# Kernel optimization log

Hardware: AMD Instinct MI355X
Metric: run time of the kernel (lower is better)

Reference implementation:

```python
import jax, jax.numpy as jnp
import numpy as np

NF4_LUT = jnp.array([-1.0, -0.6961928009986877, -0.5250730514526367, -0.39491719007492065,
                     -0.28444138169288635, -0.18477343022823334, -0.08820830285549164, 0.0,
                     0.07107656449079514, 0.14263366162776947, 0.22430233657360077,
                     0.3203405737876892, 0.4407068192958832, 0.5905631184577942,
                     0.796090841293335, 1.0], dtype=jnp.float32)

BLOCK_SIZE = 64
OUT_FEATURES = 11008
IN_FEATURES = 4096


def dequantize_nf4(packed, absmax, out_shape):
    # packed: (O, I//2) int codes 0..255; absmax: (O, num_blocks)
    higher = packed // 16
    lower = packed % 16
    unpacked = jnp.stack([lower, higher], axis=-1).reshape(out_shape)  # (O, I)
    dequant = NF4_LUT[unpacked]  # LUT gather -> fp32 (O, I)
    O, I = out_shape
    # block-wise absmax scale
    dequant = (dequant.reshape(O, I // BLOCK_SIZE, BLOCK_SIZE) * absmax[:, :, None]).reshape(O, I)
    return dequant


def setup_inputs() -> dict:
    key = jax.random.key(0)
    k1, k2, k3, k4 = jax.random.split(key, 4)
    x = jax.random.normal(k1, (4, 2048, IN_FEATURES), dtype=jnp.float32)
    weight = jax.random.randint(k2, (OUT_FEATURES, IN_FEATURES // 2), 0, 256, dtype=jnp.int32)
    absmax = jax.random.uniform(k3, (OUT_FEATURES, IN_FEATURES // BLOCK_SIZE), dtype=jnp.float32)
    bias = jax.random.normal(k4, (OUT_FEATURES,), dtype=jnp.float32)
    return {"x": x, "weight": weight, "absmax": absmax, "bias": bias}


def reference(x, weight, absmax, bias):
    w = dequantize_nf4(weight, absmax, (OUT_FEATURES, IN_FEATURES))  # (O, I)
    # F.linear: y = x @ w.T + bias
    return jnp.einsum('bsi,oi->bso', x, w) + bias
```

## Files before the change

### kernel.cpp

```cpp
#include <hip/hip_runtime.h>

#define IN_F 4096
#define OUT_F 11008

typedef __attribute__((ext_vector_type(8))) short bf16x8;
typedef __attribute__((ext_vector_type(4))) float f32x4;
typedef __attribute__((ext_vector_type(4))) unsigned short us4;
typedef __attribute__((ext_vector_type(8))) unsigned short us8;

__device__ __forceinline__ unsigned short f2bf(float f) {
  unsigned int u = __float_as_uint(f);
  u += 0x7FFFu + ((u >> 16) & 1u);
  return (unsigned short)(u >> 16);
}

__global__ __launch_bounds__(256) void cvt_x(const float* __restrict__ X,
                                             unsigned short* __restrict__ Xb, int n8) {
  for (int i = blockIdx.x * blockDim.x + threadIdx.x; i < n8;
       i += gridDim.x * blockDim.x) {
    const float4 a = reinterpret_cast<const float4*>(X)[2 * i];
    const float4 b = reinterpret_cast<const float4*>(X)[2 * i + 1];
    us8 h;
    h[0] = f2bf(a.x); h[1] = f2bf(a.y); h[2] = f2bf(a.z); h[3] = f2bf(a.w);
    h[4] = f2bf(b.x); h[5] = f2bf(b.y); h[6] = f2bf(b.z); h[7] = f2bf(b.w);
    reinterpret_cast<us8*>(Xb)[i] = h;
  }
}

__global__ __launch_bounds__(256) void dequant_w(const int* __restrict__ Wp,
                                                 const float* __restrict__ Amax,
                                                 unsigned short* __restrict__ Wb, int n4) {
  __shared__ float lutS[16];
  if (threadIdx.x < 16) {
    const float lut[16] = {-1.0f, -0.6961928009986877f, -0.5250730514526367f,
        -0.39491719007492065f, -0.28444138169288635f, -0.18477343022823334f,
        -0.08820830285549164f, 0.0f, 0.07107656449079514f, 0.14263366162776947f,
        0.22430233657360077f, 0.3203405737876892f, 0.4407068192958832f,
        0.5905631184577942f, 0.796090841293335f, 1.0f};
    lutS[threadIdx.x] = lut[threadIdx.x];
  }
  __syncthreads();
  for (int i = blockIdx.x * blockDim.x + threadIdx.x; i < n4;
       i += gridDim.x * blockDim.x) {
    const int j = i * 4;
    const int row = j >> 11;
    const int coli = j & 2047;
    const float am = Amax[row * (IN_F / 64) + (coli >> 5)];
    const int4 pk = reinterpret_cast<const int4*>(Wp)[i];
    us8 h; int c;
    c = pk.x & 255; h[0] = f2bf(lutS[c & 15] * am); h[1] = f2bf(lutS[c >> 4] * am);
    c = pk.y & 255; h[2] = f2bf(lutS[c & 15] * am); h[3] = f2bf(lutS[c >> 4] * am);
    c = pk.z & 255; h[4] = f2bf(lutS[c & 15] * am); h[5] = f2bf(lutS[c >> 4] * am);
    c = pk.w & 255; h[6] = f2bf(lutS[c & 15] * am); h[7] = f2bf(lutS[c >> 4] * am);
    reinterpret_cast<us8*>(Wb)[i] = h;
  }
}

#define MF(a, b, c) __builtin_amdgcn_mfma_f32_16x16x32_bf16(a, b, c, 0, 0, 0)
#define GLDS(src, dst) __builtin_amdgcn_global_load_lds( \
    (const __attribute__((address_space(1))) void*)(src), \
    (__attribute__((address_space(3))) void*)(dst), 16, 0, 0)
#define FENCE asm volatile("" ::: "memory")
#define BAR do { FENCE; __builtin_amdgcn_s_barrier(); FENCE; } while (0)
#define VM0 asm volatile("s_waitcnt vmcnt(0)" ::: "memory")
#define P1 __builtin_amdgcn_s_setprio(1)
#define P0 __builtin_amdgcn_s_setprio(0)

__global__ __launch_bounds__(512, 2) void gemm256(
    const unsigned short* __restrict__ A,
    const unsigned short* __restrict__ B,
    const float* __restrict__ Bias, float* __restrict__ Out, int M) {
  extern __shared__ unsigned short sm[];
  char* const smc = (char*)sm;

  const int tid = threadIdx.x;
  const int l = tid & 63;
  const int wid = tid >> 6;

  const int Nb = OUT_F / 256;

  const int bps = 16 * Nb;
  const int pxc = bps >> 3;
  const int i6 = (int)blockIdx.x % bps;
  const int sup = (int)blockIdx.x / bps;
  const int k = (i6 & 7) * pxc + (i6 >> 3);
  const int m0 = (sup * 16 + (k & 15)) * 256;
  const int n0 = (k >> 4) * 256;

  const int lv = (l & 15) * 64 + (((l >> 4) ^ ((l >> 1) & 3)) * 16);
  const int aLane = (wid >> 2) * 8192 + lv;
  const int bLane = 32768 + (wid & 3) * 4096 + lv;

  const int rq = tid >> 2;
  const int cs = (tid & 3) ^ ((tid >> 3) & 3);
  const unsigned short* gAs = A + (size_t)(m0 + rq) * IN_F + cs * 8;
  const unsigned short* gBs = B + (size_t)(n0 + rq) * IN_F + cs * 8;

#define SA(t, kh) do { \
    unsigned short* d_ = sm + (size_t)((((t) & 1) * 4096) + (kh) * 1024 + wid * 64) * 8; \
    const unsigned short* s_ = gAs + (size_t)(t) * 64 + (kh) * 32; \
    GLDS(s_, d_); GLDS(s_ + 524288, d_ + 4096); } while (0)
#define SB(t, kh) do { \
    unsigned short* d_ = sm + (size_t)((((t) & 1) * 4096) + 2048 + (kh) * 1024 + wid * 64) * 8; \
    const unsigned short* s_ = gBs + (size_t)(t) * 64 + (kh) * 32; \
    GLDS(s_, d_); GLDS(s_ + 4096, d_ + 4096); } while (0)
#undef SB
#define SB(t, kh) do { \
    unsigned short* d_ = sm + (size_t)((((t) & 1) * 4096) + 2048 + (kh) * 1024 + wid * 64) * 8; \
    const unsigned short* s_ = gBs + (size_t)(t) * 64 + (kh) * 32; \
    GLDS(s_, d_); GLDS(s_ + 524288, d_ + 4096); } while (0)

#define MM32(AA0, AA1, AA2, AA3, AA4, AA5, AA6, AA7, BB0, BB1, BB2, BB3) do { \
    acc[0][0]=MF(AA0,BB0,acc[0][0]); acc[0][1]=MF(AA0,BB1,acc[0][1]); \
    acc[0][2]=MF(AA0,BB2,acc[0][2]); acc[0][3]=MF(AA0,BB3,acc[0][3]); \
    acc[1][0]=MF(AA1,BB0,acc[1][0]); acc[1][1]=MF(AA1,BB1,acc[1][1]); \
    acc[1][2]=MF(AA1,BB2,acc[1][2]); acc[1][3]=MF(AA1,BB3,acc[1][3]); \
    acc[2][0]=MF(AA2,BB0,acc[2][0]); acc[2][1]=MF(AA2,BB1,acc[2][1]); \
    acc[2][2]=MF(AA2,BB2,acc[2][2]); acc[2][3]=MF(AA2,BB3,acc[2][3]); \
    acc[3][0]=MF(AA3,BB0,acc[3][0]); acc[3][1]=MF(AA3,BB1,acc[3][1]); \
    acc[3][2]=MF(AA3,BB2,acc[3][2]); acc[3][3]=MF(AA3,BB3,acc[3][3]); \
    acc[4][0]=MF(AA4,BB0,acc[4][0]); acc[4][1]=MF(AA4,BB1,acc[4][1]); \
    acc[4][2]=MF(AA4,BB2,acc[4][2]); acc[4][3]=MF(AA4,BB3,acc[4][3]); \
    acc[5][0]=MF(AA5,BB0,acc[5][0]); acc[5][1]=MF(AA5,BB1,acc[5][1]); \
    acc[5][2]=MF(AA5,BB2,acc[5][2]); acc[5][3]=MF(AA5,BB3,acc[5][3]); \
    acc[6][0]=MF(AA6,BB0,acc[6][0]); acc[6][1]=MF(AA6,BB1,acc[6][1]); \
    acc[6][2]=MF(AA6,BB2,acc[6][2]); acc[6][3]=MF(AA6,BB3,acc[6][3]); \
    acc[7][0]=MF(AA7,BB0,acc[7][0]); acc[7][1]=MF(AA7,BB1,acc[7][1]); \
    acc[7][2]=MF(AA7,BB2,acc[7][2]); acc[7][3]=MF(AA7,BB3,acc[7][3]); } while (0)

#define KTILE(T, STG) do { \
    VM0; \
    BAR; \
    const char* LAb = smc + (((T) & 1) << 16) + aLane; \
    const char* LBb = smc + (((T) & 1) << 16) + bLane; \
    bf16x8 x0, x1, x2, x3, x4, x5, x6, x7, y0, y1, y2, y3; \
    bf16x8 u0, u1, u2, u3, u4, u5, u6, u7, v0, v1, v2, v3; \
    y0 = *(const bf16x8*)(LBb);        y1 = *(const bf16x8*)(LBb + 1024); \
    y2 = *(const bf16x8*)(LBb + 2048); y3 = *(const bf16x8*)(LBb + 3072); \
    x0 = *(const bf16x8*)(LAb);        x1 = *(const bf16x8*)(LAb + 1024); \
    x2 = *(const bf16x8*)(LAb + 2048); x3 = *(const bf16x8*)(LAb + 3072); \
    x4 = *(const bf16x8*)(LAb + 4096); x5 = *(const bf16x8*)(LAb + 5120); \
    x6 = *(const bf16x8*)(LAb + 6144); x7 = *(const bf16x8*)(LAb + 7168); \
    v0 = *(const bf16x8*)(LBb + 16384);        v1 = *(const bf16x8*)(LBb + 16384 + 1024); \
    v2 = *(const bf16x8*)(LBb + 16384 + 2048); v3 = *(const bf16x8*)(LBb + 16384 + 3072); \
    u0 = *(const bf16x8*)(LAb + 16384);        u1 = *(const bf16x8*)(LAb + 16384 + 1024); \
    u2 = *(const bf16x8*)(LAb + 16384 + 2048); u3 = *(const bf16x8*)(LAb + 16384 + 3072); \
    u4 = *(const bf16x8*)(LAb + 16384 + 4096); u5 = *(const bf16x8*)(LAb + 16384 + 5120); \
    u6 = *(const bf16x8*)(LAb + 16384 + 6144); u7 = *(const bf16x8*)(LAb + 16384 + 7168); \
    if (STG) { SA((T) + 1, 0); SB((T) + 1, 0); SA((T) + 1, 1); SB((T) + 1, 1); } \
    P1; MM32(x0, x1, x2, x3, x4, x5, x6, x7, y0, y1, y2, y3); P0; \
    P1; MM32(u0, u1, u2, u3, u4, u5, u6, u7, v0, v1, v2, v3); P0; \
  } while (0)

  f32x4 acc[8][4];
#pragma unroll
  for (int i = 0; i < 8; ++i)
#pragma unroll
    for (int j = 0; j < 4; ++j) acc[i][j] = {0.f, 0.f, 0.f, 0.f};

  SA(0, 0); SB(0, 0); SA(0, 1); SB(0, 1);

  for (int T = 0; T < 63; ++T) { KTILE(T, 1); }
  KTILE(63, 0);

  const int crow = m0 + (wid >> 2) * 128 + ((l >> 4) << 2);
  const int ccol = n0 + (wid & 3) * 64 + (l & 15);
#pragma unroll
  for (int nf = 0; nf < 4; ++nf) {
    const float bv = Bias[ccol + nf * 16];
#pragma unroll
    for (int f = 0; f < 8; ++f)
#pragma unroll
      for (int rg = 0; rg < 4; ++rg)
        Out[(size_t)(crow + f * 16 + rg) * OUT_F + ccol + nf * 16] = acc[f][nf][rg] + bv;
  }
}

__global__ __launch_bounds__(256, 2) void nf4_gemm_fused(
    const float* __restrict__ X, const int* __restrict__ Wp,
    const float* __restrict__ Amax, const float* __restrict__ Bias,
    float* __restrict__ Out, int M) {
  __shared__ unsigned short As[128 * 64];
  __shared__ unsigned short Bs[128 * 64];
  __shared__ float lutS[16];

  const int t = threadIdx.x;
  const int l = t & 63;
  const int wid = t >> 6;

  if (t < 16) {
    const float lut[16] = {-1.0f, -0.6961928009986877f, -0.5250730514526367f,
        -0.39491719007492065f, -0.28444138169288635f, -0.18477343022823334f,
        -0.08820830285549164f, 0.0f, 0.07107656449079514f, 0.14263366162776947f,
        0.22430233657360077f, 0.3203405737876892f, 0.4407068192958832f,
        0.5905631184577942f, 0.796090841293335f, 1.0f};
    lutS[t] = lut[t];
  }

  const int ntile = OUT_F / 128;
  const int m0 = (blockIdx.x / ntile) * 128;
  const int n0 = (blockIdx.x % ntile) * 128;

  const int ar = t >> 4;
  const int ac4 = t & 15;
  const int br = t >> 3;
  const int bg = t & 7;
  const int wm = (wid >> 1) * 64;
  const int wn = (wid & 1) * 64;

  f32x4 acc[4][4];
#pragma unroll
  for (int i = 0; i < 4; ++i)
#pragma unroll
    for (int j = 0; j < 4; ++j) acc[i][j] = {0.f, 0.f, 0.f, 0.f};

  __syncthreads();

  for (int k0 = 0; k0 < IN_F; k0 += 64) {
#pragma unroll
    for (int p = 0; p < 8; ++p) {
      const int r = p * 16 + ar;
      const float4 v = *reinterpret_cast<const float4*>(
          X + (size_t)(m0 + r) * IN_F + k0 + ac4 * 4);
      us4 h;
      h[0] = f2bf(v.x); h[1] = f2bf(v.y); h[2] = f2bf(v.z); h[3] = f2bf(v.w);
      const int byte = r * 128 + ((ac4 * 8) ^ ((r & 7) << 4));
      *reinterpret_cast<us4*>(reinterpret_cast<char*>(As) + byte) = h;
    }
#pragma unroll
    for (int p = 0; p < 4; ++p) {
      const int r = p * 32 + br;
      const float amv = Amax[(size_t)(n0 + r) * (IN_F / 64) + (k0 >> 6)];
      const int4 pk = *reinterpret_cast<const int4*>(
          Wp + (size_t)(n0 + r) * (IN_F / 2) + (k0 >> 1) + bg * 4);
      us8 h;
      {
        int c;
        c = pk.x & 255; h[0] = f2bf(lutS[c & 15] * amv); h[1] = f2bf(lutS[c >> 4] * amv);
        c = pk.y & 255; h[2] = f2bf(lutS[c & 15] * amv); h[3] = f2bf(lutS[c >> 4] * amv);
        c = pk.z & 255; h[4] = f2bf(lutS[c & 15] * amv); h[5] = f2bf(lutS[c >> 4] * amv);
        c = pk.w & 255; h[6] = f2bf(lutS[c & 15] * amv); h[7] = f2bf(lutS[c >> 4] * amv);
      }
      const int byte = r * 128 + ((bg * 16) ^ ((r & 7) << 4));
      *reinterpret_cast<us8*>(reinterpret_cast<char*>(Bs) + byte) = h;
    }
    __syncthreads();

#pragma unroll
    for (int kk = 0; kk < 64; kk += 32) {
      bf16x8 af[4], bfv[4];
      const int kb = (kk + ((l >> 4) << 3)) * 2;
#pragma unroll
      for (int i = 0; i < 4; ++i) {
        const int row = wm + i * 16 + (l & 15);
        af[i] = *reinterpret_cast<const bf16x8*>(
            reinterpret_cast<const char*>(As) + row * 128 + (kb ^ ((row & 7) << 4)));
      }
#pragma unroll
      for (int j = 0; j < 4; ++j) {
        const int row = wn + j * 16 + (l & 15);
        bfv[j] = *reinterpret_cast<const bf16x8*>(
            reinterpret_cast<const char*>(Bs) + row * 128 + (kb ^ ((row & 7) << 4)));
      }
#pragma unroll
      for (int i = 0; i < 4; ++i)
#pragma unroll
        for (int j = 0; j < 4; ++j)
          acc[i][j] = __builtin_amdgcn_mfma_f32_16x16x32_bf16(af[i], bfv[j], acc[i][j], 0, 0, 0);
    }
    __syncthreads();
  }

  const int crow0 = m0 + wm + ((l >> 4) << 2);
  const int ccol0 = n0 + wn + (l & 15);
#pragma unroll
  for (int j = 0; j < 4; ++j) {
    const float bv = Bias[ccol0 + j * 16];
#pragma unroll
    for (int i = 0; i < 4; ++i)
#pragma unroll
      for (int rg = 0; rg < 4; ++rg)
        Out[(size_t)(crow0 + i * 16 + rg) * OUT_F + ccol0 + j * 16] = acc[i][j][rg] + bv;
  }
}

extern "C" void kernel_launch(void* const* d_in, const int* in_sizes, int n_in,
                              void* d_out, int out_size, void* d_ws, size_t ws_size,
                              hipStream_t stream) {
  const float* X = (const float*)d_in[0];
  const int* Wp = (const int*)d_in[1];
  const float* Amax = (const float*)d_in[2];
  const float* Bias = (const float*)d_in[3];
  float* Out = (float*)d_out;

  const int M = in_sizes[0] / IN_F;
  const size_t needX = (size_t)M * IN_F * 2;
  const size_t needW = (size_t)OUT_F * IN_F * 2;
  const int grid256 = (M / 256) * (OUT_F / 256);

  if (ws_size >= needX + needW && (M % 4096) == 0) {
    unsigned short* Xb = (unsigned short*)d_ws;
    unsigned short* Wb = Xb + (size_t)M * IN_F;
    (void)hipFuncSetAttribute(reinterpret_cast<const void*>(gemm256),
                              hipFuncAttributeMaxDynamicSharedMemorySize, 131072);
    cvt_x<<<2048, 256, 0, stream>>>(X, Xb, M * (IN_F / 8));
    dequant_w<<<2048, 256, 0, stream>>>(Wp, Amax, Wb, OUT_F * (IN_F / 8));
    gemm256<<<grid256, 512, 131072, stream>>>(Xb, Wb, Bias, Out, M);
  } else {
    const int grid = (M / 128) * (OUT_F / 128);
    nf4_gemm_fused<<<grid, 256, 0, stream>>>(X, Wp, Amax, Bias, Out, M);
  }
}
```

Before: 866.6 us.

## Interleave LDS reads, global-to-LDS staging and MFMA in four sub-phases per k-tile

```diff
diff --git a/kernel.cpp b/kernel.cpp
--- a/kernel.cpp
+++ b/kernel.cpp
@@ -62,6 +62,7 @@
     (__attribute__((address_space(3))) void*)(dst), 16, 0, 0)
 #define FENCE asm volatile("" ::: "memory")
 #define BAR do { FENCE; __builtin_amdgcn_s_barrier(); FENCE; } while (0)
+#define VM4 asm volatile("s_waitcnt vmcnt(4)" ::: "memory")
 #define VM0 asm volatile("s_waitcnt vmcnt(0)" ::: "memory")
 #define P1 __builtin_amdgcn_s_setprio(1)
 #define P0 __builtin_amdgcn_s_setprio(0)
@@ -103,53 +104,46 @@
 #define SB(t, kh) do { \
     unsigned short* d_ = sm + (size_t)((((t) & 1) * 4096) + 2048 + (kh) * 1024 + wid * 64) * 8; \
     const unsigned short* s_ = gBs + (size_t)(t) * 64 + (kh) * 32; \
-    GLDS(s_, d_); GLDS(s_ + 4096, d_ + 4096); } while (0)
-#undef SB
-#define SB(t, kh) do { \
-    unsigned short* d_ = sm + (size_t)((((t) & 1) * 4096) + 2048 + (kh) * 1024 + wid * 64) * 8; \
-    const unsigned short* s_ = gBs + (size_t)(t) * 64 + (kh) * 32; \
     GLDS(s_, d_); GLDS(s_ + 524288, d_ + 4096); } while (0)
 
-#define MM32(AA0, AA1, AA2, AA3, AA4, AA5, AA6, AA7, BB0, BB1, BB2, BB3) do { \
-    acc[0][0]=MF(AA0,BB0,acc[0][0]); acc[0][1]=MF(AA0,BB1,acc[0][1]); \
-    acc[0][2]=MF(AA0,BB2,acc[0][2]); acc[0][3]=MF(AA0,BB3,acc[0][3]); \
-    acc[1][0]=MF(AA1,BB0,acc[1][0]); acc[1][1]=MF(AA1,BB1,acc[1][1]); \
-    acc[1][2]=MF(AA1,BB2,acc[1][2]); acc[1][3]=MF(AA1,BB3,acc[1][3]); \
-    acc[2][0]=MF(AA2,BB0,acc[2][0]); acc[2][1]=MF(AA2,BB1,acc[2][1]); \
-    acc[2][2]=MF(AA2,BB2,acc[2][2]); acc[2][3]=MF(AA2,BB3,acc[2][3]); \
-    acc[3][0]=MF(AA3,BB0,acc[3][0]); acc[3][1]=MF(AA3,BB1,acc[3][1]); \
-    acc[3][2]=MF(AA3,BB2,acc[3][2]); acc[3][3]=MF(AA3,BB3,acc[3][3]); \
-    acc[4][0]=MF(AA4,BB0,acc[4][0]); acc[4][1]=MF(AA4,BB1,acc[4][1]); \
-    acc[4][2]=MF(AA4,BB2,acc[4][2]); acc[4][3]=MF(AA4,BB3,acc[4][3]); \
-    acc[5][0]=MF(AA5,BB0,acc[5][0]); acc[5][1]=MF(AA5,BB1,acc[5][1]); \
-    acc[5][2]=MF(AA5,BB2,acc[5][2]); acc[5][3]=MF(AA5,BB3,acc[5][3]); \
-    acc[6][0]=MF(AA6,BB0,acc[6][0]); acc[6][1]=MF(AA6,BB1,acc[6][1]); \
-    acc[6][2]=MF(AA6,BB2,acc[6][2]); acc[6][3]=MF(AA6,BB3,acc[6][3]); \
-    acc[7][0]=MF(AA7,BB0,acc[7][0]); acc[7][1]=MF(AA7,BB1,acc[7][1]); \
-    acc[7][2]=MF(AA7,BB2,acc[7][2]); acc[7][3]=MF(AA7,BB3,acc[7][3]); } while (0)
-
-#define KTILE(T, STG) do { \
-    VM0; \
-    BAR; \
+#define MMQ(A0, A1, A2, A3, mb) do { \
+    acc[(mb)+0][0]=MF(A0,y0,acc[(mb)+0][0]); acc[(mb)+0][1]=MF(A0,y1,acc[(mb)+0][1]); \
+    acc[(mb)+0][2]=MF(A0,y2,acc[(mb)+0][2]); acc[(mb)+0][3]=MF(A0,y3,acc[(mb)+0][3]); \
+    acc[(mb)+1][0]=MF(A1,y0,acc[(mb)+1][0]); acc[(mb)+1][1]=MF(A1,y1,acc[(mb)+1][1]); \
+    acc[(mb)+1][2]=MF(A1,y2,acc[(mb)+1][2]); acc[(mb)+1][3]=MF(A1,y3,acc[(mb)+1][3]); \
+    acc[(mb)+2][0]=MF(A2,y0,acc[(mb)+2][0]); acc[(mb)+2][1]=MF(A2,y1,acc[(mb)+2][1]); \
+    acc[(mb)+2][2]=MF(A2,y2,acc[(mb)+2][2]); acc[(mb)+2][3]=MF(A2,y3,acc[(mb)+2][3]); \
+    acc[(mb)+3][0]=MF(A3,y0,acc[(mb)+3][0]); acc[(mb)+3][1]=MF(A3,y1,acc[(mb)+3][1]); \
+    acc[(mb)+3][2]=MF(A3,y2,acc[(mb)+3][2]); acc[(mb)+3][3]=MF(A3,y3,acc[(mb)+3][3]); } while (0)
+
+#define KTILE(T, STG, VMW) do { \
     const char* LAb = smc + (((T) & 1) << 16) + aLane; \
     const char* LBb = smc + (((T) & 1) << 16) + bLane; \
     bf16x8 x0, x1, x2, x3, x4, x5, x6, x7, y0, y1, y2, y3; \
-    bf16x8 u0, u1, u2, u3, u4, u5, u6, u7, v0, v1, v2, v3; \
+     \
     y0 = *(const bf16x8*)(LBb);        y1 = *(const bf16x8*)(LBb + 1024); \
     y2 = *(const bf16x8*)(LBb + 2048); y3 = *(const bf16x8*)(LBb + 3072); \
     x0 = *(const bf16x8*)(LAb);        x1 = *(const bf16x8*)(LAb + 1024); \
     x2 = *(const bf16x8*)(LAb + 2048); x3 = *(const bf16x8*)(LAb + 3072); \
+    if (STG) SA((T) + 1, 0); \
+    BAR; P1; MMQ(x0, x1, x2, x3, 0); P0; BAR; \
+     \
     x4 = *(const bf16x8*)(LAb + 4096); x5 = *(const bf16x8*)(LAb + 5120); \
     x6 = *(const bf16x8*)(LAb + 6144); x7 = *(const bf16x8*)(LAb + 7168); \
-    v0 = *(const bf16x8*)(LBb + 16384);        v1 = *(const bf16x8*)(LBb + 16384 + 1024); \
-    v2 = *(const bf16x8*)(LBb + 16384 + 2048); v3 = *(const bf16x8*)(LBb + 16384 + 3072); \
-    u0 = *(const bf16x8*)(LAb + 16384);        u1 = *(const bf16x8*)(LAb + 16384 + 1024); \
-    u2 = *(const bf16x8*)(LAb + 16384 + 2048); u3 = *(const bf16x8*)(LAb + 16384 + 3072); \
-    u4 = *(const bf16x8*)(LAb + 16384 + 4096); u5 = *(const bf16x8*)(LAb + 16384 + 5120); \
-    u6 = *(const bf16x8*)(LAb + 16384 + 6144); u7 = *(const bf16x8*)(LAb + 16384 + 7168); \
-    if (STG) { SA((T) + 1, 0); SB((T) + 1, 0); SA((T) + 1, 1); SB((T) + 1, 1); } \
-    P1; MM32(x0, x1, x2, x3, x4, x5, x6, x7, y0, y1, y2, y3); P0; \
-    P1; MM32(u0, u1, u2, u3, u4, u5, u6, u7, v0, v1, v2, v3); P0; \
+    if (STG) SB((T) + 1, 0); \
+    BAR; P1; MMQ(x4, x5, x6, x7, 4); P0; VMW; BAR; \
+     \
+    y0 = *(const bf16x8*)(LBb + 16384);        y1 = *(const bf16x8*)(LBb + 16384 + 1024); \
+    y2 = *(const bf16x8*)(LBb + 16384 + 2048); y3 = *(const bf16x8*)(LBb + 16384 + 3072); \
+    x0 = *(const bf16x8*)(LAb + 16384);        x1 = *(const bf16x8*)(LAb + 16384 + 1024); \
+    x2 = *(const bf16x8*)(LAb + 16384 + 2048); x3 = *(const bf16x8*)(LAb + 16384 + 3072); \
+    if (STG) SA((T) + 1, 1); \
+    BAR; P1; MMQ(x0, x1, x2, x3, 0); P0; BAR; \
+     \
+    x4 = *(const bf16x8*)(LAb + 16384 + 4096); x5 = *(const bf16x8*)(LAb + 16384 + 5120); \
+    x6 = *(const bf16x8*)(LAb + 16384 + 6144); x7 = *(const bf16x8*)(LAb + 16384 + 7168); \
+    if (STG) SB((T) + 1, 1); \
+    BAR; P1; MMQ(x4, x5, x6, x7, 4); P0; VMW; BAR; \
   } while (0)
 
   f32x4 acc[8][4];
@@ -159,9 +153,11 @@
     for (int j = 0; j < 4; ++j) acc[i][j] = {0.f, 0.f, 0.f, 0.f};
 
   SA(0, 0); SB(0, 0); SA(0, 1); SB(0, 1);
-
-  for (int T = 0; T < 63; ++T) { KTILE(T, 1); }
-  KTILE(63, 0);
+  VM4;
+  BAR;
+
+  for (int T = 0; T < 63; ++T) { KTILE(T, 1, VM4); }
+  KTILE(63, 0, VM0);
 
   const int crow = m0 + (wid >> 2) * 128 + ((l >> 4) << 2);
   const int ccol = n0 + (wid & 3) * 64 + (l & 15);
```

Result: faster. 805.4 us (-7.1%).

## Replace 256x256 GEMM tile with 128x128 tile and interleaved staging loads

Applied to the files above, without the earlier changes.

```diff
diff --git a/kernel.cpp b/kernel.cpp
--- a/kernel.cpp
+++ b/kernel.cpp
@@ -66,113 +66,104 @@
 #define P1 __builtin_amdgcn_s_setprio(1)
 #define P0 __builtin_amdgcn_s_setprio(0)
 
-__global__ __launch_bounds__(512, 2) void gemm256(
+__global__ __launch_bounds__(256, 2) void gemm128(
     const unsigned short* __restrict__ A,
     const unsigned short* __restrict__ B,
     const float* __restrict__ Bias, float* __restrict__ Out, int M) {
   extern __shared__ unsigned short sm[];
-  char* const smc = (char*)sm;
+  unsigned short* const As = sm;
+  unsigned short* const Bs = sm + 16384;
 
   const int tid = threadIdx.x;
   const int l = tid & 63;
   const int wid = tid >> 6;
 
-  const int Nb = OUT_F / 256;
-
-  const int bps = 16 * Nb;
+  const int Nb = OUT_F / 128;
+  const int bps = 32 * Nb;
   const int pxc = bps >> 3;
   const int i6 = (int)blockIdx.x % bps;
   const int sup = (int)blockIdx.x / bps;
   const int k = (i6 & 7) * pxc + (i6 >> 3);
-  const int m0 = (sup * 16 + (k & 15)) * 256;
-  const int n0 = (k >> 4) * 256;
-
-  const int lv = (l & 15) * 64 + (((l >> 4) ^ ((l >> 1) & 3)) * 16);
-  const int aLane = (wid >> 2) * 8192 + lv;
-  const int bLane = 32768 + (wid & 3) * 4096 + lv;
-
-  const int rq = tid >> 2;
-  const int cs = (tid & 3) ^ ((tid >> 3) & 3);
-  const unsigned short* gAs = A + (size_t)(m0 + rq) * IN_F + cs * 8;
-  const unsigned short* gBs = B + (size_t)(n0 + rq) * IN_F + cs * 8;
-
-#define SA(t, kh) do { \
-    unsigned short* d_ = sm + (size_t)((((t) & 1) * 4096) + (kh) * 1024 + wid * 64) * 8; \
-    const unsigned short* s_ = gAs + (size_t)(t) * 64 + (kh) * 32; \
-    GLDS(s_, d_); GLDS(s_ + 524288, d_ + 4096); } while (0)
-#define SB(t, kh) do { \
-    unsigned short* d_ = sm + (size_t)((((t) & 1) * 4096) + 2048 + (kh) * 1024 + wid * 64) * 8; \
-    const unsigned short* s_ = gBs + (size_t)(t) * 64 + (kh) * 32; \
-    GLDS(s_, d_); GLDS(s_ + 4096, d_ + 4096); } while (0)
-#undef SB
-#define SB(t, kh) do { \
-    unsigned short* d_ = sm + (size_t)((((t) & 1) * 4096) + 2048 + (kh) * 1024 + wid * 64) * 8; \
-    const unsigned short* s_ = gBs + (size_t)(t) * 64 + (kh) * 32; \
-    GLDS(s_, d_); GLDS(s_ + 524288, d_ + 4096); } while (0)
-
-#define MM32(AA0, AA1, AA2, AA3, AA4, AA5, AA6, AA7, BB0, BB1, BB2, BB3) do { \
-    acc[0][0]=MF(AA0,BB0,acc[0][0]); acc[0][1]=MF(AA0,BB1,acc[0][1]); \
-    acc[0][2]=MF(AA0,BB2,acc[0][2]); acc[0][3]=MF(AA0,BB3,acc[0][3]); \
-    acc[1][0]=MF(AA1,BB0,acc[1][0]); acc[1][1]=MF(AA1,BB1,acc[1][1]); \
-    acc[1][2]=MF(AA1,BB2,acc[1][2]); acc[1][3]=MF(AA1,BB3,acc[1][3]); \
-    acc[2][0]=MF(AA2,BB0,acc[2][0]); acc[2][1]=MF(AA2,BB1,acc[2][1]); \
-    acc[2][2]=MF(AA2,BB2,acc[2][2]); acc[2][3]=MF(AA2,BB3,acc[2][3]); \
-    acc[3][0]=MF(AA3,BB0,acc[3][0]); acc[3][1]=MF(AA3,BB1,acc[3][1]); \
-    acc[3][2]=MF(AA3,BB2,acc[3][2]); acc[3][3]=MF(AA3,BB3,acc[3][3]); \
-    acc[4][0]=MF(AA4,BB0,acc[4][0]); acc[4][1]=MF(AA4,BB1,acc[4][1]); \
-    acc[4][2]=MF(AA4,BB2,acc[4][2]); acc[4][3]=MF(AA4,BB3,acc[4][3]); \
-    acc[5][0]=MF(AA5,BB0,acc[5][0]); acc[5][1]=MF(AA5,BB1,acc[5][1]); \
-    acc[5][2]=MF(AA5,BB2,acc[5][2]); acc[5][3]=MF(AA5,BB3,acc[5][3]); \
-    acc[6][0]=MF(AA6,BB0,acc[6][0]); acc[6][1]=MF(AA6,BB1,acc[6][1]); \
-    acc[6][2]=MF(AA6,BB2,acc[6][2]); acc[6][3]=MF(AA6,BB3,acc[6][3]); \
-    acc[7][0]=MF(AA7,BB0,acc[7][0]); acc[7][1]=MF(AA7,BB1,acc[7][1]); \
-    acc[7][2]=MF(AA7,BB2,acc[7][2]); acc[7][3]=MF(AA7,BB3,acc[7][3]); } while (0)
+  const int m0 = (sup * 32 + (k & 31)) * 128;
+  const int n0 = (k >> 5) * 128;
+
+  const int wm = (wid >> 1) * 64;
+  const int wn = (wid & 1) * 64;
+
+  const int srow = wid * 8 + (l >> 3);
+  const int schunk = ((l & 7) ^ (l >> 3)) * 8;
+  const unsigned short* gA = A + (size_t)(m0 + srow) * IN_F + schunk;
+  const unsigned short* gB = B + (size_t)(n0 + srow) * IN_F + schunk;
+
+#define SA4(t) do { const int bb = ((t) & 1) * 8192; const size_t ko = (size_t)(t) * 64; \
+    GLDS(gA + ko,                      As + bb + (wid * 8) * 64); \
+    GLDS(gA + ko + (size_t)32 * IN_F,  As + bb + (32 + wid * 8) * 64); \
+    GLDS(gA + ko + (size_t)64 * IN_F,  As + bb + (64 + wid * 8) * 64); \
+    GLDS(gA + ko + (size_t)96 * IN_F,  As + bb + (96 + wid * 8) * 64); } while (0)
+#define SB4(t) do { const int bb = ((t) & 1) * 8192; const size_t ko = (size_t)(t) * 64; \
+    GLDS(gB + ko,                      Bs + bb + (wid * 8) * 64); \
+    GLDS(gB + ko + (size_t)32 * IN_F,  Bs + bb + (32 + wid * 8) * 64); \
+    GLDS(gB + ko + (size_t)64 * IN_F,  Bs + bb + (64 + wid * 8) * 64); \
+    GLDS(gB + ko + (size_t)96 * IN_F,  Bs + bb + (96 + wid * 8) * 64); } while (0)
+
+  const int xorv = (l & 7) << 4;
+  const int kb0 = (((l >> 4) * 8) * 2) ^ xorv;
+  const int kb1 = ((32 + (l >> 4) * 8) * 2) ^ xorv;
+  const int arow = (wm + (l & 15)) * 128;
+  const int brow = (wn + (l & 15)) * 128;
+
+#define MM16(A0, A1, A2, A3, B0, B1, B2, B3) do { \
+    acc[0][0]=MF(A0,B0,acc[0][0]); acc[0][1]=MF(A0,B1,acc[0][1]); \
+    acc[0][2]=MF(A0,B2,acc[0][2]); acc[0][3]=MF(A0,B3,acc[0][3]); \
+    acc[1][0]=MF(A1,B0,acc[1][0]); acc[1][1]=MF(A1,B1,acc[1][1]); \
+    acc[1][2]=MF(A1,B2,acc[1][2]); acc[1][3]=MF(A1,B3,acc[1][3]); \
+    acc[2][0]=MF(A2,B0,acc[2][0]); acc[2][1]=MF(A2,B1,acc[2][1]); \
+    acc[2][2]=MF(A2,B2,acc[2][2]); acc[2][3]=MF(A2,B3,acc[2][3]); \
+    acc[3][0]=MF(A3,B0,acc[3][0]); acc[3][1]=MF(A3,B1,acc[3][1]); \
+    acc[3][2]=MF(A3,B2,acc[3][2]); acc[3][3]=MF(A3,B3,acc[3][3]); } while (0)
 
 #define KTILE(T, STG) do { \
     VM0; \
     BAR; \
-    const char* LAb = smc + (((T) & 1) << 16) + aLane; \
-    const char* LBb = smc + (((T) & 1) << 16) + bLane; \
-    bf16x8 x0, x1, x2, x3, x4, x5, x6, x7, y0, y1, y2, y3; \
-    bf16x8 u0, u1, u2, u3, u4, u5, u6, u7, v0, v1, v2, v3; \
-    y0 = *(const bf16x8*)(LBb);        y1 = *(const bf16x8*)(LBb + 1024); \
-    y2 = *(const bf16x8*)(LBb + 2048); y3 = *(const bf16x8*)(LBb + 3072); \
-    x0 = *(const bf16x8*)(LAb);        x1 = *(const bf16x8*)(LAb + 1024); \
-    x2 = *(const bf16x8*)(LAb + 2048); x3 = *(const bf16x8*)(LAb + 3072); \
-    x4 = *(const bf16x8*)(LAb + 4096); x5 = *(const bf16x8*)(LAb + 5120); \
-    x6 = *(const bf16x8*)(LAb + 6144); x7 = *(const bf16x8*)(LAb + 7168); \
-    v0 = *(const bf16x8*)(LBb + 16384);        v1 = *(const bf16x8*)(LBb + 16384 + 1024); \
-    v2 = *(const bf16x8*)(LBb + 16384 + 2048); v3 = *(const bf16x8*)(LBb + 16384 + 3072); \
-    u0 = *(const bf16x8*)(LAb + 16384);        u1 = *(const bf16x8*)(LAb + 16384 + 1024); \
-    u2 = *(const bf16x8*)(LAb + 16384 + 2048); u3 = *(const bf16x8*)(LAb + 16384 + 3072); \
-    u4 = *(const bf16x8*)(LAb + 16384 + 4096); u5 = *(const bf16x8*)(LAb + 16384 + 5120); \
-    u6 = *(const bf16x8*)(LAb + 16384 + 6144); u7 = *(const bf16x8*)(LAb + 16384 + 7168); \
-    if (STG) { SA((T) + 1, 0); SB((T) + 1, 0); SA((T) + 1, 1); SB((T) + 1, 1); } \
-    P1; MM32(x0, x1, x2, x3, x4, x5, x6, x7, y0, y1, y2, y3); P0; \
-    P1; MM32(u0, u1, u2, u3, u4, u5, u6, u7, v0, v1, v2, v3); P0; \
+    const char* Ab = (const char*)As + ((T) & 1) * 16384; \
+    const char* Bb = (const char*)Bs + ((T) & 1) * 16384; \
+    bf16x8 a0, a1, a2, a3, b0, b1, b2, b3; \
+    bf16x8 c0, c1, c2, c3, d0, d1, d2, d3; \
+    a0 = *(const bf16x8*)(Ab + arow + kb0);        a1 = *(const bf16x8*)(Ab + arow + 2048 + kb0); \
+    a2 = *(const bf16x8*)(Ab + arow + 4096 + kb0); a3 = *(const bf16x8*)(Ab + arow + 6144 + kb0); \
+    b0 = *(const bf16x8*)(Bb + brow + kb0);        b1 = *(const bf16x8*)(Bb + brow + 2048 + kb0); \
+    b2 = *(const bf16x8*)(Bb + brow + 4096 + kb0); b3 = *(const bf16x8*)(Bb + brow + 6144 + kb0); \
+    if (STG) SA4((T) + 1); \
+    c0 = *(const bf16x8*)(Ab + arow + kb1);        c1 = *(const bf16x8*)(Ab + arow + 2048 + kb1); \
+    c2 = *(const bf16x8*)(Ab + arow + 4096 + kb1); c3 = *(const bf16x8*)(Ab + arow + 6144 + kb1); \
+    d0 = *(const bf16x8*)(Bb + brow + kb1);        d1 = *(const bf16x8*)(Bb + brow + 2048 + kb1); \
+    d2 = *(const bf16x8*)(Bb + brow + 4096 + kb1); d3 = *(const bf16x8*)(Bb + brow + 6144 + kb1); \
+    P1; MM16(a0, a1, a2, a3, b0, b1, b2, b3); P0; \
+    if (STG) SB4((T) + 1); \
+    P1; MM16(c0, c1, c2, c3, d0, d1, d2, d3); P0; \
   } while (0)
 
-  f32x4 acc[8][4];
-#pragma unroll
-  for (int i = 0; i < 8; ++i)
+  f32x4 acc[4][4];
+#pragma unroll
+  for (int i = 0; i < 4; ++i)
 #pragma unroll
     for (int j = 0; j < 4; ++j) acc[i][j] = {0.f, 0.f, 0.f, 0.f};
 
-  SA(0, 0); SB(0, 0); SA(0, 1); SB(0, 1);
+  SA4(0); SB4(0);
 
   for (int T = 0; T < 63; ++T) { KTILE(T, 1); }
   KTILE(63, 0);
 
-  const int crow = m0 + (wid >> 2) * 128 + ((l >> 4) << 2);
-  const int ccol = n0 + (wid & 3) * 64 + (l & 15);
-#pragma unroll
-  for (int nf = 0; nf < 4; ++nf) {
-    const float bv = Bias[ccol + nf * 16];
-#pragma unroll
-    for (int f = 0; f < 8; ++f)
+  const int crow0 = m0 + wm + ((l >> 4) << 2);
+  const int ccol0 = n0 + wn + (l & 15);
+#pragma unroll
+  for (int j = 0; j < 4; ++j) {
+    const float bv = Bias[ccol0 + j * 16];
+#pragma unroll
+    for (int i = 0; i < 4; ++i)
 #pragma unroll
       for (int rg = 0; rg < 4; ++rg)
-        Out[(size_t)(crow + f * 16 + rg) * OUT_F + ccol + nf * 16] = acc[f][nf][rg] + bv;
+        Out[(size_t)(crow0 + i * 16 + rg) * OUT_F + ccol0 + j * 16] = acc[i][j][rg] + bv;
   }
 }
 
@@ -296,18 +287,17 @@
   const int M = in_sizes[0] / IN_F;
   const size_t needX = (size_t)M * IN_F * 2;
   const size_t needW = (size_t)OUT_F * IN_F * 2;
-  const int grid256 = (M / 256) * (OUT_F / 256);
+  const int grid = (M / 128) * (OUT_F / 128);
 
   if (ws_size >= needX + needW && (M % 4096) == 0) {
     unsigned short* Xb = (unsigned short*)d_ws;
     unsigned short* Wb = Xb + (size_t)M * IN_F;
-    (void)hipFuncSetAttribute(reinterpret_cast<const void*>(gemm256),
-                              hipFuncAttributeMaxDynamicSharedMemorySize, 131072);
+    (void)hipFuncSetAttribute(reinterpret_cast<const void*>(gemm128),
+                              hipFuncAttributeMaxDynamicSharedMemorySize, 65536);
     cvt_x<<<2048, 256, 0, stream>>>(X, Xb, M * (IN_F / 8));
     dequant_w<<<2048, 256, 0, stream>>>(Wp, Amax, Wb, OUT_F * (IN_F / 8));
-    gemm256<<<grid256, 512, 131072, stream>>>(Xb, Wb, Bias, Out, M);
+    gemm128<<<grid, 256, 65536, stream>>>(Xb, Wb, Bias, Out, M);
   } else {
-    const int grid = (M / 128) * (OUT_F / 128);
     nf4_gemm_fused<<<grid, 256, 0, stream>>>(X, Wp, Amax, Bias, Out, M);
   }
 }
```

Result: slower. 1.004 ms (+15.9%).
